# Performance work log

Hardware: AMD Instinct MI355X
Metric: run time of the kernel (lower is better)

The kernel has to match this reference:

```python
import jax, jax.numpy as jnp
import numpy as np

N = 100000          # nodes
E = 800000          # edges per relation
R = 6               # relations
B = 1000            # graphs
IN_DIM = 14
POS_COL = 5
PE = 8              # pos_emb_dim
H = 128             # hidden_dim
OUT = 128           # out_dim
NPOS = 24
D1 = IN_DIM - 1 + PE  # 21, GAT layer-1 input dim


def setup_inputs() -> dict:
    key = jax.random.key(0)
    ks = jax.random.split(key, 20)
    x_all = jax.random.normal(ks[0], (N, IN_DIM), dtype=jnp.float32)
    pos = jax.random.randint(ks[1], (N,), 0, NPOS)
    x_all = x_all.at[:, POS_COL].set(pos.astype(jnp.float32))
    edges = jax.random.randint(ks[2], (R, 2, E), 0, N, dtype=jnp.int32)
    batch = jnp.sort(jax.random.randint(ks[3], (N,), 0, B, dtype=jnp.int32))
    pos_table = jax.random.normal(ks[4], (NPOS, PE), dtype=jnp.float32) * 0.02
    W1 = jax.random.normal(ks[5], (R, D1, H), dtype=jnp.float32) * 0.1
    as1 = jax.random.normal(ks[6], (R, H), dtype=jnp.float32) * 0.1
    ad1 = jax.random.normal(ks[7], (R, H), dtype=jnp.float32) * 0.1
    b1 = jnp.zeros((R, H), dtype=jnp.float32)
    W2 = jax.random.normal(ks[8], (R, H, H), dtype=jnp.float32) * 0.05
    as2 = jax.random.normal(ks[9], (R, H), dtype=jnp.float32) * 0.1
    ad2 = jax.random.normal(ks[10], (R, H), dtype=jnp.float32) * 0.1
    b2 = jnp.zeros((R, H), dtype=jnp.float32)
    n1w = jnp.ones((H,), dtype=jnp.float32)
    n1b = jnp.zeros((H,), dtype=jnp.float32)
    n2w = jnp.ones((H,), dtype=jnp.float32)
    n2b = jnp.zeros((H,), dtype=jnp.float32)
    query = jax.random.normal(ks[11], (H,), dtype=jnp.float32) * 0.02
    projW = jax.random.normal(ks[12], (H, OUT), dtype=jnp.float32) * 0.05
    projb = jnp.zeros((OUT,), dtype=jnp.float32)
    return dict(x_all=x_all, edges=edges, batch=batch, pos_table=pos_table,
                W1=W1, as1=as1, ad1=ad1, b1=b1, W2=W2, as2=as2, ad2=ad2, b2=b2,
                n1w=n1w, n1b=n1b, n2w=n2w, n2b=n2b, query=query, projW=projW, projb=projb)


def _seg_softmax(logits, seg, num):
    m = jax.lax.stop_gradient(jax.ops.segment_max(logits, seg, num_segments=num))
    e = jnp.exp(logits - m[seg])
    s = jax.ops.segment_sum(e, seg, num_segments=num)
    return e / s[seg]


def _gat_layer(x, W, a_s, a_d, b, edges):
    # sum over R relation-specific GATConv(heads=1, concat=False) outputs
    n = x.shape[0]
    out = jnp.zeros((n, W.shape[-1]), dtype=x.dtype)
    for r in range(R):
        xp = x @ W[r]                       # [N, H] projected features
        src, dst = edges[r, 0], edges[r, 1]
        z = (xp @ a_s[r])[src] + (xp @ a_d[r])[dst]
        z = jnp.where(z > 0, z, 0.2 * z)    # LeakyReLU(0.2)
        alpha = _seg_softmax(z, dst, n)     # per-destination softmax
        agg = jax.ops.segment_sum(alpha[:, None] * xp[src], dst, num_segments=n)
        out = out + agg + b[r]
    return out


def _ln(x, w, b):
    mu = x.mean(-1, keepdims=True)
    v = ((x - mu) ** 2).mean(-1, keepdims=True)
    return (x - mu) / jnp.sqrt(v + 1e-5) * w + b


def reference(x_all, edges, batch, pos_table, W1, as1, ad1, b1,
              W2, as2, ad2, b2, n1w, n1b, n2w, n2b, query, projW, projb):
    cont = jnp.concatenate([x_all[:, :POS_COL], x_all[:, POS_COL + 1:]], axis=1)
    pidx = jnp.clip(x_all[:, POS_COL].astype(jnp.int32), 0, NPOS - 1)
    x = jnp.concatenate([cont, pos_table[pidx]], axis=1)  # [N, D1]
    x = _gat_layer(x, W1, as1, ad1, b1, edges)
    x = _ln(jax.nn.gelu(x, approximate=False), n1w, n1b)
    x = _gat_layer(x, W2, as2, ad2, b2, edges)
    x = _ln(jax.nn.gelu(x, approximate=False), n2w, n2b)
    # AttentionPooling: gather-score-softmax-scatter over batch segments
    scores = x @ query
    w = _seg_softmax(scores, batch, B)
    pool = jax.ops.segment_sum(w[:, None] * x, batch, num_segments=B)  # [B, H]
    return pool @ projW + projb
```

## Files before the change

kernel.cpp:

```cpp
#include <hip/hip_runtime.h>
#include <math.h>

#define NN   100000
#define EE   800000
#define RR   6
#define BB   1000
#define HH   128
#define MM   (RR*NN)
#define NBPR ((NN + 255) >> 8)
#define NBK  (RR * NBPR)
#define CH   4096
#define CAP  4096

static inline int ceil_div(int a, int b){ return (a+b-1)/b; }

typedef __attribute__((ext_vector_type(8))) short bf16x8;
typedef __attribute__((ext_vector_type(4))) short bf16x4;
typedef __attribute__((ext_vector_type(4))) float f32x4;

__device__ __forceinline__ unsigned fenc(float f){
  unsigned u = __float_as_uint(f);
  return (u & 0x80000000u) ? ~u : (u | 0x80000000u);
}
__device__ __forceinline__ float fdec(unsigned u){
  return __uint_as_float((u & 0x80000000u) ? (u & 0x7fffffffu) : ~u);
}
__device__ __forceinline__ unsigned short f2bf(float f){
  unsigned u = __float_as_uint(f);
  return (unsigned short)((u + 0x7fffu + ((u >> 16) & 1u)) >> 16);
}
__device__ __forceinline__ float bf2f(unsigned short h){
  return __uint_as_float(((unsigned)h) << 16);
}

__global__ void k_binscatter(const int* __restrict__ edges, int* __restrict__ bcur,
                             unsigned* __restrict__ ebkt)
{
  __shared__ int hist[NBPR];
  __shared__ int base[NBPR];
  int t = threadIdx.x;
  const int nch = (EE + CH - 1) / CH;
  int r = blockIdx.x / nch, c = blockIdx.x - r*nch;
  for (int i = t; i < NBPR; i += 256) hist[i] = 0;
  __syncthreads();
  const int* sptr = edges + (size_t)r*2*EE;
  const int* dptr = sptr + EE;
  int e0 = c*CH, e1 = min(EE, e0 + CH);
  for (int i = e0 + t; i < e1; i += 256)
    atomicAdd(&hist[dptr[i] >> 8], 1);
  __syncthreads();
  for (int i = t; i < NBPR; i += 256) {
    int h = hist[i];
    int gb = r*NBPR + i;
    base[i] = h ? (gb*CAP + atomicAdd(&bcur[gb], h)) : 0;
    hist[i] = 0;
  }
  __syncthreads();
  for (int i = e0 + t; i < e1; i += 256) {
    int dst = dptr[i];
    int b = dst >> 8;
    int slot = base[b] + atomicAdd(&hist[b], 1);
    ebkt[slot] = ((unsigned)sptr[i] << 8) | (unsigned)(dst & 255);
  }
}

__global__ void k_bscan(const int* __restrict__ bcur, int* __restrict__ boff,
                        int* __restrict__ off)
{
  __shared__ int sh[256];
  int t = threadIdx.x;
  int carry = 0;
  for (int c = 0; c < NBK; c += 256) {
    int idx = c + t;
    int v = (idx < NBK) ? bcur[idx] : 0;
    sh[t] = v;
    __syncthreads();
    for (int o = 1; o < 256; o <<= 1) {
      int add = (t >= o) ? sh[t-o] : 0;
      __syncthreads();
      sh[t] += add;
      __syncthreads();
    }
    int incl = sh[t];
    int tot  = sh[255];
    if (idx < NBK) boff[idx] = carry + incl - v;
    __syncthreads();
    carry += tot;
  }
  if (t == 0) { boff[NBK] = carry; off[MM] = carry; }
}

__global__ void k_bbuild(const unsigned* __restrict__ ebkt, const int* __restrict__ bcur,
                         const int* __restrict__ boff,
                         int* __restrict__ off, int* __restrict__ elist)
{
  __shared__ int cnt[256];
  __shared__ int sc[256];
  __shared__ int cur[256];
  int t = threadIdx.x;
  int bb = blockIdx.x;
  int e0r = bb*CAP, e1r = e0r + bcur[bb];
  int w0 = boff[bb];
  cnt[t] = 0;
  __syncthreads();
  for (int i = e0r + t; i < e1r; i += 256)
    atomicAdd(&cnt[ebkt[i] & 255u], 1);
  __syncthreads();
  sc[t] = cnt[t];
  __syncthreads();
  for (int o = 1; o < 256; o <<= 1) {
    int add = (t >= o) ? sc[t-o] : 0;
    __syncthreads();
    sc[t] += add;
    __syncthreads();
  }
  int excl = sc[t] - cnt[t];
  int r = bb / NBPR, b = bb - r*NBPR;
  int dst = b*256 + t;
  if (dst < NN) off[r*NN + dst] = w0 + excl;
  cur[t] = w0 + excl;
  __syncthreads();
  for (int i = e0r + t; i < e1r; i += 256) {
    unsigned w = ebkt[i];
    int slot = atomicAdd(&cur[w & 255u], 1);
    elist[slot] = (int)(w >> 8);
  }
}

__global__ void k_featprep(const float* __restrict__ x_all, const float* __restrict__ pos_table,
                           short* __restrict__ x0h, short* __restrict__ x0l)
{
  int gid = blockIdx.x*256 + threadIdx.x;
  if (gid >= NN*32) return;
  int nidx = gid >> 5, c = gid & 31;
  float v = 0.f;
  if (c < 13) {
    int scl = (c < 5) ? c : c + 1;
    v = x_all[nidx*14 + scl];
  } else if (c < 21) {
    int pi = (int)x_all[nidx*14 + 5];
    pi = pi < 0 ? 0 : (pi > 23 ? 23 : pi);
    v = pos_table[pi*8 + (c - 13)];
  }
  unsigned short h = f2bf(v);
  unsigned short l = f2bf(v - bf2f(h));
  x0h[gid] = (short)h;
  x0l[gid] = (short)l;
}

template<int KP>
__global__ void k_wprep(const float* __restrict__ W, int K,
                        short* __restrict__ Wh, short* __restrict__ Wl)
{
  int gid = blockIdx.x*256 + threadIdx.x;
  if (gid >= RR*128*KP) return;
  int r = gid / (128*KP);
  int rem = gid - r*(128*KP);
  int nn = rem / KP, k = rem - nn*KP;
  float v = (k < K) ? W[((size_t)r*K + k)*128 + nn] : 0.f;
  unsigned short h = f2bf(v);
  unsigned short l = f2bf(v - bf2f(h));
  Wh[gid] = (short)h;
  Wl[gid] = (short)l;
}

__global__ void k_wprep2(const float* __restrict__ W,
                         short* __restrict__ Wh, short* __restrict__ Wl)
{
  int gid = blockIdx.x*256 + threadIdx.x;
  if (gid >= RR*128*128) return;
  int r = gid / (128*128);
  int i = gid - r*(128*128);
  int kc = i >> 12;
  int lg = (i >> 10) & 3;
  int row = (i >> 3) & 127;
  int e = i & 7;
  int k = kc*32 + 16*(e >> 2) + 4*lg + (e & 3);
  float v = W[((size_t)r*128 + k)*128 + row];
  unsigned short h = f2bf(v);
  unsigned short l = f2bf(v - bf2f(h));
  Wh[gid] = (short)h;
  Wl[gid] = (short)l;
}

template<int KP>
__global__ void k_wa(const float* __restrict__ W, const float* __restrict__ as,
                     const float* __restrict__ ad, int K, float* __restrict__ wa)
{
  int idx = blockIdx.x*256 + threadIdx.x;
  if (idx >= 12*KP) return;
  int rr = idx / KP, k = idx - rr*KP;
  int r = (rr < 6) ? rr : rr - 6;
  const float* a = ((rr < 6) ? as : ad) + (size_t)r*HH;
  float s = 0.f;
  if (k < K) {
    const float* wrow = W + ((size_t)r*K + k)*128;
    #pragma unroll 8
    for (int h = 0; h < 128; ++h) s = fmaf(wrow[h], a[h], s);
  }
  wa[idx] = s;
}

__global__ void k_zsd32(const short* __restrict__ xh, const short* __restrict__ xl,
                        const float* __restrict__ wa, float* __restrict__ zsd, int n)
{
  __shared__ float w[12*32];
  int tid = threadIdx.x;
  for (int i = tid; i < 12*32; i += 256) w[i] = wa[i];
  __syncthreads();
  int g = blockIdx.x*256 + tid;
  if (g >= n) return;
  float v[32];
  #pragma unroll
  for (int c = 0; c < 4; ++c) {
    uint4 vh = *(const uint4*)(xh + (size_t)g*32 + c*8);
    uint4 vl = *(const uint4*)(xl + (size_t)g*32 + c*8);
    const unsigned short* hp = (const unsigned short*)&vh;
    const unsigned short* lp = (const unsigned short*)&vl;
    #pragma unroll
    for (int j = 0; j < 8; ++j) v[c*8+j] = bf2f(hp[j]) + bf2f(lp[j]);
  }
  #pragma unroll
  for (int rr = 0; rr < 12; ++rr) {
    float d = 0.f;
    #pragma unroll
    for (int k = 0; k < 32; ++k) d = fmaf(v[k], w[rr*32+k], d);
    zsd[(size_t)rr*n + g] = d;
  }
}

__global__ void k_zsd128(const unsigned short* __restrict__ xh,
                         const float* __restrict__ wa, float* __restrict__ zsd, int n)
{
  __shared__ float w[12*128];
  int tid = threadIdx.x;
  for (int i = tid; i < 12*128; i += 256) w[i] = wa[i];
  __syncthreads();
  int gid = blockIdx.x*256 + tid;
  int g = gid >> 4, l = tid & 15;
  if (g >= n) return;
  uint4 vh = *(const uint4*)(xh + (size_t)g*128 + l*8);
  const unsigned short* hp = (const unsigned short*)&vh;
  float v[8];
  #pragma unroll
  for (int j = 0; j < 8; ++j) v[j] = bf2f(hp[j]);
  float dot[12];
  #pragma unroll
  for (int rr = 0; rr < 12; ++rr) {
    float p = 0.f;
    #pragma unroll
    for (int j = 0; j < 8; ++j) p = fmaf(v[j], w[rr*128 + l*8 + j], p);
    p += __shfl_xor(p, 1); p += __shfl_xor(p, 2);
    p += __shfl_xor(p, 4); p += __shfl_xor(p, 8);
    dot[rr] = p;
  }
  if (l < 12) zsd[(size_t)l*n + g] = dot[l];
}

__global__ void k_agg1(const unsigned short* __restrict__ x0h, const float* __restrict__ zsd,
                       const int* __restrict__ elist, const int* __restrict__ off,
                       unsigned short* __restrict__ aggH, unsigned short* __restrict__ aggL,
                       int n)
{
  int gid = blockIdx.x*256 + threadIdx.x;
  int g = gid >> 4;
  int l = threadIdx.x & 15;
  if (g >= n) return;
  int sub = l >> 2, ch = l & 3;

  for (int rel = 0; rel < RR; ++rel) {
    const float* zsr = zsd + (size_t)rel*n;
    const float* zdr = zsd + (size_t)(6+rel)*n;
    int o0 = off[(size_t)rel*NN + g];
    int deg = off[(size_t)rel*NN + g + 1] - o0;
    float acc[8] = {0,0,0,0,0,0,0,0};
    float inv = 0.f;
    if (deg > 0) {
      float zdd = zdr[g];
      float m = -3.4e38f, es = 0.f;
      for (int i = l; i < deg; i += 16) {
        float z = zsr[elist[o0+i]] + zdd;
        z = (z > 0.f) ? z : 0.2f*z;
        float mn = fmaxf(m, z);
        es = es*__expf(m - mn) + __expf(z - mn);
        m = mn;
      }
      #pragma unroll
      for (int o = 1; o <= 8; o <<= 1) {
        float mo = __shfl_xor(m, o), eo = __shfl_xor(es, o);
        float mn = fmaxf(m, mo);
        es = es*__expf(m - mn) + eo*__expf(mo - mn);
        m = mn;
      }
      inv = 1.f / es;
      for (int base = 0; base < deg; base += 8) {
        int i0 = base + sub, i1 = base + 4 + sub;
        float e0 = 0.f, e1 = 0.f; int s0 = 0, s1 = 0;
        if (i0 < deg) {
          s0 = elist[o0+i0];
          float z = zsr[s0] + zdd;
          z = (z > 0.f) ? z : 0.2f*z;
          e0 = __expf(z - m);
        }
        if (i1 < deg) {
          s1 = elist[o0+i1];
          float z = zsr[s1] + zdd;
          z = (z > 0.f) ? z : 0.2f*z;
          e1 = __expf(z - m);
        }
        uint4 v0 = *(const uint4*)(x0h + (size_t)s0*32 + ch*8);
        uint4 v1 = *(const uint4*)(x0h + (size_t)s1*32 + ch*8);
        acc[0] = fmaf(e0, __uint_as_float(v0.x << 16),         acc[0]);
        acc[1] = fmaf(e0, __uint_as_float(v0.x & 0xffff0000u), acc[1]);
        acc[2] = fmaf(e0, __uint_as_float(v0.y << 16),         acc[2]);
        acc[3] = fmaf(e0, __uint_as_float(v0.y & 0xffff0000u), acc[3]);
        acc[4] = fmaf(e0, __uint_as_float(v0.z << 16),         acc[4]);
        acc[5] = fmaf(e0, __uint_as_float(v0.z & 0xffff0000u), acc[5]);
        acc[6] = fmaf(e0, __uint_as_float(v0.w << 16),         acc[6]);
        acc[7] = fmaf(e0, __uint_as_float(v0.w & 0xffff0000u), acc[7]);
        acc[0] = fmaf(e1, __uint_as_float(v1.x << 16),         acc[0]);
        acc[1] = fmaf(e1, __uint_as_float(v1.x & 0xffff0000u), acc[1]);
        acc[2] = fmaf(e1, __uint_as_float(v1.y << 16),         acc[2]);
        acc[3] = fmaf(e1, __uint_as_float(v1.y & 0xffff0000u), acc[3]);
        acc[4] = fmaf(e1, __uint_as_float(v1.z << 16),         acc[4]);
        acc[5] = fmaf(e1, __uint_as_float(v1.z & 0xffff0000u), acc[5]);
        acc[6] = fmaf(e1, __uint_as_float(v1.w << 16),         acc[6]);
        acc[7] = fmaf(e1, __uint_as_float(v1.w & 0xffff0000u), acc[7]);
      }
      #pragma unroll
      for (int j = 0; j < 8; ++j) {
        acc[j] += __shfl_xor(acc[j], 4);
        acc[j] += __shfl_xor(acc[j], 8);
      }
    }
    if (sub == 0) {
      uint4 ph, pl;
      unsigned* php = (unsigned*)&ph; unsigned* plp = (unsigned*)&pl;
      #pragma unroll
      for (int j2 = 0; j2 < 4; ++j2) {
        float a0 = acc[2*j2]   * inv;
        float a1 = acc[2*j2+1] * inv;
        unsigned short h0 = f2bf(a0), h1 = f2bf(a1);
        php[j2] = ((unsigned)h1 << 16) | h0;
        plp[j2] = ((unsigned)f2bf(a1 - bf2f(h1)) << 16) | f2bf(a0 - bf2f(h0));
      }
      size_t o = ((size_t)rel*n + g)*32 + ch*8;
      *(uint4*)(aggH + o) = ph;
      *(uint4*)(aggL + o) = pl;
    }
  }
}

__device__ __forceinline__ bf16x8 ldfragG(const short* __restrict__ p, int row, int kb, int KP_)
{
  bf16x4 a = *(const bf16x4*)(p + (size_t)row*KP_ + kb);
  bf16x4 b = *(const bf16x4*)(p + (size_t)row*KP_ + kb + 16);
  return __builtin_shufflevector(a, b, 0,1,2,3,4,5,6,7);
}

__global__ __launch_bounds__(256, 4)
void k_gemm1(const short* __restrict__ aggH, const short* __restrict__ aggL,
             const short* __restrict__ Wh, const short* __restrict__ Wl,
             const float* __restrict__ bsv,
             const float* __restrict__ nw, const float* __restrict__ nb,
             unsigned short* __restrict__ Yh, int n)
{
  __shared__ __align__(16) float Cs[32*136];
  int tid = threadIdx.x;
  int r0 = blockIdx.x * 32;
  int wid = tid >> 6, lane = tid & 63;
  int lr = lane & 15, lg = lane >> 4;
  int rt = wid >> 1;
  int c0 = (wid & 1) * 4;
  int arow = r0 + rt*16 + lr;
  int kb = 4*lg;
  f32x4 acct[4] = {{0,0,0,0},{0,0,0,0},{0,0,0,0},{0,0,0,0}};

  for (int rel = 0; rel < RR; ++rel) {
    const short* Ahr = aggH + (size_t)rel*n*32;
    const short* Alr = aggL + (size_t)rel*n*32;
    const short* Whr = Wh + (size_t)rel*128*32;
    const short* Wlr = Wl + (size_t)rel*128*32;
    bf16x8 ah = ldfragG(Ahr, arow, kb, 32);
    bf16x8 al = ldfragG(Alr, arow, kb, 32);
    #pragma unroll
    for (int t = 0; t < 4; ++t) {
      int wrow = (c0 + t)*16 + lr;
      bf16x8 whf = ldfragG(Whr, wrow, kb, 32);
      bf16x8 wlf = ldfragG(Wlr, wrow, kb, 32);
      acct[t] = __builtin_amdgcn_mfma_f32_16x16x32_bf16(ah, whf, acct[t], 0, 0, 0);
      acct[t] = __builtin_amdgcn_mfma_f32_16x16x32_bf16(al, whf, acct[t], 0, 0, 0);
      acct[t] = __builtin_amdgcn_mfma_f32_16x16x32_bf16(ah, wlf, acct[t], 0, 0, 0);
    }
  }

  #pragma unroll
  for (int t = 0; t < 4; ++t)
    #pragma unroll
    for (int v = 0; v < 4; ++v) {
      int row = rt*16 + lg*4 + v;
      int col = (c0 + t)*16 + lr;
      float x = acct[t][v] + bsv[col];
      Cs[row*136 + col] = 0.5f*x*(1.f + erff(x*0.70710678118654752f));
    }
  __syncthreads();
  {
    int r = tid >> 3, sg = tid & 7;
    float vals[16];
    float s = 0.f;
    #pragma unroll
    for (int i = 0; i < 16; ++i) { vals[i] = Cs[r*136 + sg*16 + i]; s += vals[i]; }
    s += __shfl_xor(s, 1); s += __shfl_xor(s, 2); s += __shfl_xor(s, 4);
    float mu = s * (1.f/128.f);
    float var = 0.f;
    #pragma unroll
    for (int i = 0; i < 16; ++i) { vals[i] -= mu; var += vals[i]*vals[i]; }
    var += __shfl_xor(var, 1); var += __shfl_xor(var, 2); var += __shfl_xor(var, 4);
    float inv = 1.f / sqrtf(var*(1.f/128.f) + 1e-5f);
    int g = r0 + r;
    uint4 ph0, ph1;
    unsigned* php0 = (unsigned*)&ph0; unsigned* php1 = (unsigned*)&ph1;
    #pragma unroll
    for (int j2 = 0; j2 < 8; ++j2) {
      int c = sg*16 + 2*j2;
      float y0 = vals[2*j2]  *inv*nw[c]   + nb[c];
      float y1 = vals[2*j2+1]*inv*nw[c+1] + nb[c+1];
      unsigned hw = ((unsigned)f2bf(y1) << 16) | f2bf(y0);
      if (j2 < 4) php0[j2] = hw; else php1[j2-4] = hw;
    }
    *(uint4*)(Yh + (size_t)g*128 + sg*16)     = ph0;
    *(uint4*)(Yh + (size_t)g*128 + sg*16 + 8) = ph1;
  }
}

#define ACC8(W_, U_) \
  tmp[0] = fmaf(W_, __uint_as_float((U_).x << 16),         tmp[0]); \
  tmp[1] = fmaf(W_, __uint_as_float((U_).x & 0xffff0000u), tmp[1]); \
  tmp[2] = fmaf(W_, __uint_as_float((U_).y << 16),         tmp[2]); \
  tmp[3] = fmaf(W_, __uint_as_float((U_).y & 0xffff0000u), tmp[3]); \
  tmp[4] = fmaf(W_, __uint_as_float((U_).z << 16),         tmp[4]); \
  tmp[5] = fmaf(W_, __uint_as_float((U_).z & 0xffff0000u), tmp[5]); \
  tmp[6] = fmaf(W_, __uint_as_float((U_).w << 16),         tmp[6]); \
  tmp[7] = fmaf(W_, __uint_as_float((U_).w & 0xffff0000u), tmp[7]);

__global__ void k_agg2(const unsigned short* __restrict__ h1,
                       const float* __restrict__ zsd,
                       const int* __restrict__ elist,
                       const int* __restrict__ off,
                       int rbase,
                       unsigned short* __restrict__ agg2,
                       int n)
{
  int gid = blockIdx.x*256 + threadIdx.x;
  int g = gid >> 4;
  int l = threadIdx.x & 15;
  int gbase = threadIdx.x & 48;
  if (g >= n) return;

  for (int r = 0; r < 3; ++r) {
    int o0 = off[(size_t)r*NN + g], o1 = off[(size_t)r*NN + g + 1];
    int deg = o1 - o0;
    float tmp[8] = {0,0,0,0,0,0,0,0};
    float inv = 0.f;
    if (deg > 0) {
      const float* zsr = zsd + (size_t)(rbase+r)*n;
      float zdd = zsd[(size_t)(6+rbase+r)*n + g];

      float m = -3.4e38f;
      for (int i = l; i < deg; i += 16) {
        float z = zsr[elist[o0+i]] + zdd;
        z = (z > 0.f) ? z : 0.2f*z;
        m = fmaxf(m, z);
      }
      m = fmaxf(m, __shfl_xor(m, 1));
      m = fmaxf(m, __shfl_xor(m, 2));
      m = fmaxf(m, __shfl_xor(m, 4));
      m = fmaxf(m, __shfl_xor(m, 8));

      float esum = 0.f;
      for (int base = 0; base < deg; base += 16) {
        int i = base + l;
        float ew = 0.f; int s = 0;
        if (i < deg) {
          s = elist[o0+i];
          float z = zsr[s] + zdd;
          z = (z > 0.f) ? z : 0.2f*z;
          ew = __expf(z - m);
        }
        esum += ew;
        int cnt = min(16, deg - base);
        for (int t = 0; t < cnt; t += 4) {
          float w0 = __shfl(ew, gbase + t);
          float w1 = __shfl(ew, gbase + t + 1);
          float w2 = __shfl(ew, gbase + t + 2);
          float w3 = __shfl(ew, gbase + t + 3);
          int a0 = __shfl(s, gbase + t);
          int a1 = __shfl(s, gbase + t + 1);
          int a2 = __shfl(s, gbase + t + 2);
          int a3 = __shfl(s, gbase + t + 3);
          uint4 u0 = *(const uint4*)(h1 + (size_t)a0*128 + l*8);
          uint4 u1 = *(const uint4*)(h1 + (size_t)a1*128 + l*8);
          uint4 u2 = *(const uint4*)(h1 + (size_t)a2*128 + l*8);
          uint4 u3 = *(const uint4*)(h1 + (size_t)a3*128 + l*8);
          ACC8(w0, u0);
          ACC8(w1, u1);
          ACC8(w2, u2);
          ACC8(w3, u3);
        }
      }
      esum += __shfl_xor(esum, 1);
      esum += __shfl_xor(esum, 2);
      esum += __shfl_xor(esum, 4);
      esum += __shfl_xor(esum, 8);
      inv = 1.f / esum;
    }
    uint4 ph;
    unsigned* php = (unsigned*)&ph;
    #pragma unroll
    for (int j2 = 0; j2 < 4; ++j2) {
      float a0 = tmp[2*j2]   * inv;
      float a1 = tmp[2*j2+1] * inv;
      php[j2] = ((unsigned)f2bf(a1) << 16) | f2bf(a0);
    }
    *(uint4*)(agg2 + ((size_t)r*n + g)*128 + l*8) = ph;
  }
}

template<int FIN>
__global__ __launch_bounds__(512, 2)
void k_gemm2(const unsigned short* __restrict__ agg2,
             const short* __restrict__ WhAll, const short* __restrict__ WlAll, int rbase,
             const float* __restrict__ bsv,
             const float* __restrict__ nw, const float* __restrict__ nb,
             float* __restrict__ hacc, float* __restrict__ Yf,
             const float* __restrict__ q, const int* __restrict__ batch,
             float* __restrict__ scores, unsigned* __restrict__ bmax, int n)
{
  constexpr int KP = 128;
  __shared__ __align__(16) short lds[2*128*KP];
  constexpr int WH0 = 0, WL0 = 128*KP;
  int tid = threadIdx.x;
  int r0 = blockIdx.x * 128;
  int wid = tid >> 6, lane = tid & 63;
  int lr = lane & 15, lg = lane >> 4;
  int grow = r0 + wid*16 + lr;
  int growc = min(grow, n-1);
  f32x4 acc[8] = {{0,0,0,0},{0,0,0,0},{0,0,0,0},{0,0,0,0},
                  {0,0,0,0},{0,0,0,0},{0,0,0,0},{0,0,0,0}};

  for (int rel = 0; rel < 3; ++rel) {
    const short* Ar = (const short*)(agg2 + (size_t)rel*n*KP);
    const short* Wh = WhAll + (size_t)(rbase+rel)*128*KP;
    const short* Wl = WlAll + (size_t)(rbase+rel)*128*KP;
    for (int ch = tid; ch < 128*16; ch += 512) {
      *(bf16x8*)(lds + WH0 + ch*8) = *(const bf16x8*)(Wh + (size_t)ch*8);
      *(bf16x8*)(lds + WL0 + ch*8) = *(const bf16x8*)(Wl + (size_t)ch*8);
    }
    __syncthreads();
    #pragma unroll
    for (int kc = 0; kc < 4; ++kc) {
      int kb = kc*32 + 4*lg;
      bf16x8 ah = ldfragG(Ar, growc, kb, KP);
      int fbase = ((kc*4 + lg)*128)*8;
      #pragma unroll
      for (int ct = 0; ct < 8; ++ct) {
        int wrow = ct*16 + lr;
        bf16x8 wh = *(const bf16x8*)(lds + WH0 + fbase + wrow*8);
        bf16x8 wl = *(const bf16x8*)(lds + WL0 + fbase + wrow*8);
        acc[ct] = __builtin_amdgcn_mfma_f32_16x16x32_bf16(ah, wh, acc[ct], 0, 0, 0);
        acc[ct] = __builtin_amdgcn_mfma_f32_16x16x32_bf16(ah, wl, acc[ct], 0, 0, 0);
      }
    }
    __syncthreads();
  }

  if (FIN == 0) {
    #pragma unroll
    for (int v = 0; v < 4; ++v) {
      int row = r0 + wid*16 + lg*4 + v;
      if (row < n) {
        #pragma unroll
        for (int ct = 0; ct < 8; ++ct)
          hacc[(size_t)row*128 + ct*16 + lr] = acc[ct][v];
      }
    }
  } else {
    #pragma unroll
    for (int v = 0; v < 4; ++v) {
      int row = r0 + wid*16 + lg*4 + v;
      int rowc = min(row, n-1);
      float vals[8];
      float s = 0.f;
      #pragma unroll
      for (int ct = 0; ct < 8; ++ct) {
        int c = ct*16 + lr;
        float x = acc[ct][v] + hacc[(size_t)rowc*128 + c] + bsv[c];
        x = 0.5f*x*(1.f + erff(x*0.70710678118654752f));
        vals[ct] = x;
        s += x;
      }
      s += __shfl_xor(s, 1); s += __shfl_xor(s, 2);
      s += __shfl_xor(s, 4); s += __shfl_xor(s, 8);
      float mu = s * (1.f/128.f);
      float var = 0.f;
      #pragma unroll
      for (int ct = 0; ct < 8; ++ct) { vals[ct] -= mu; var += vals[ct]*vals[ct]; }
      var += __shfl_xor(var, 1); var += __shfl_xor(var, 2);
      var += __shfl_xor(var, 4); var += __shfl_xor(var, 8);
      float inv = 1.f / sqrtf(var*(1.f/128.f) + 1e-5f);
      float sc = 0.f;
      #pragma unroll
      for (int ct = 0; ct < 8; ++ct) {
        int c = ct*16 + lr;
        float y = vals[ct]*inv*nw[c] + nb[c];
        if (row < n) Yf[(size_t)row*128 + c] = y;
        sc = fmaf(y, q[c], sc);
      }
      sc += __shfl_xor(sc, 1); sc += __shfl_xor(sc, 2);
      sc += __shfl_xor(sc, 4); sc += __shfl_xor(sc, 8);
      if (lr == 0 && row < n) {
        scores[row] = sc;
        atomicMax(&bmax[batch[row]], fenc(sc));
      }
    }
  }
}

__global__ void k_bsum(const float* __restrict__ b, float* __restrict__ bs)
{
  int t = threadIdx.x;
  float s = 0.f;
  #pragma unroll
  for (int r = 0; r < RR; ++r) s += b[r*HH + t];
  bs[t] = s;
}

__global__ void k_segbounds(const int* __restrict__ batch, int* __restrict__ segst,
                            int n, int numB)
{
  int b = blockIdx.x*256 + threadIdx.x;
  if (b > numB) return;
  int lo = 0, hi = n;
  while (lo < hi) { int mid = (lo+hi) >> 1; if (batch[mid] < b) lo = mid+1; else hi = mid; }
  segst[b] = lo;
}

__global__ void k_pool(const float* __restrict__ X, const float* __restrict__ scores,
                       const int* __restrict__ segst, const unsigned* __restrict__ bmax,
                       float* __restrict__ pool, int numB)
{
  int b = blockIdx.x;
  int t = threadIdx.x;
  int s0 = segst[b], s1 = segst[b+1];
  float m = fdec(bmax[b]);
  float acc0 = 0.f, acc1 = 0.f, esum = 0.f;
  int i = s0;
  for (; i + 1 < s1; i += 2) {
    float e0 = __expf(scores[i] - m);
    float e1 = __expf(scores[i+1] - m);
    esum += e0 + e1;
    acc0 = fmaf(e0, X[(size_t)i*128 + t], acc0);
    acc1 = fmaf(e1, X[(size_t)(i+1)*128 + t], acc1);
  }
  if (i < s1) {
    float e0 = __expf(scores[i] - m);
    esum += e0;
    acc0 = fmaf(e0, X[(size_t)i*128 + t], acc0);
  }
  float inv = (s1 > s0) ? 1.f/esum : 0.f;
  pool[(size_t)b*128 + t] = (acc0 + acc1) * inv;
}

__global__ void k_outgemm(const float* __restrict__ pool, const float* __restrict__ projW,
                          const float* __restrict__ projb, float* __restrict__ out, int numB)
{
  int b = blockIdx.x;
  int j = threadIdx.x;
  __shared__ float p[128];
  p[j] = pool[(size_t)b*128 + j];
  __syncthreads();
  float acc = projb[j];
  #pragma unroll 16
  for (int k = 0; k < 128; ++k) acc = fmaf(p[k], projW[(size_t)k*128 + j], acc);
  out[(size_t)b*128 + j] = acc;
}

extern "C" void kernel_launch(void* const* d_in, const int* in_sizes, int n_in,
                              void* d_out, int out_size, void* d_ws, size_t ws_size,
                              hipStream_t stream)
{
  const float* x_all = (const float*)d_in[0];
  const int*   edges = (const int*)d_in[1];
  const int*   batch = (const int*)d_in[2];
  const float* pos_table = (const float*)d_in[3];
  const float* W1  = (const float*)d_in[4];
  const float* as1 = (const float*)d_in[5];
  const float* ad1 = (const float*)d_in[6];
  const float* b1  = (const float*)d_in[7];
  const float* W2  = (const float*)d_in[8];
  const float* as2 = (const float*)d_in[9];
  const float* ad2 = (const float*)d_in[10];
  const float* b2  = (const float*)d_in[11];
  const float* n1w = (const float*)d_in[12];
  const float* n1b = (const float*)d_in[13];
  const float* n2w = (const float*)d_in[14];
  const float* n2b = (const float*)d_in[15];
  const float* query = (const float*)d_in[16];
  const float* projW = (const float*)d_in[17];
  const float* projb = (const float*)d_in[18];
  float* out = (float*)d_out;
  (void)in_sizes; (void)n_in; (void)out_size; (void)ws_size;

  char* p = (char*)d_ws;
  auto alloc = [&](size_t b){ void* r = (void*)p; p += (b + 255) & ~(size_t)255; return r; };
  int*   off   = (int*)alloc((size_t)(MM+1)*sizeof(int));
  int*   elist = (int*)alloc((size_t)RR*EE*sizeof(int));
  int*   boff  = (int*)alloc((size_t)(NBK+1)*sizeof(int));
  int*   bcur  = (int*)alloc((size_t)NBK*sizeof(int));
  short* wtH   = (short*)alloc((size_t)RR*128*128*sizeof(short));
  short* wtL   = (short*)alloc((size_t)RR*128*128*sizeof(short));
  float* wa    = (float*)alloc((size_t)12*128*sizeof(float));
  float* zsd   = (float*)alloc((size_t)12*NN*sizeof(float));
  float* bsv   = (float*)alloc(128*sizeof(float));
  int*   segst = (int*)alloc((size_t)(BB+1)*sizeof(int));
  unsigned* bmax = (unsigned*)alloc((size_t)BB*sizeof(unsigned));
  float* pool  = (float*)alloc((size_t)BB*HH*sizeof(float));
  float* scrs  = (float*)alloc((size_t)NN*sizeof(float));
  unsigned short* big = (unsigned short*)alloc((size_t)3*NN*128*sizeof(short));
  float* R1    = (float*)alloc((size_t)NN*128*sizeof(float));
  float* R2    = (float*)alloc((size_t)NN*128*sizeof(float));

  unsigned* ebkt = (unsigned*)R1;
  short* x0h = (short*)R1;
  short* x0l = x0h + (size_t)NN*32;
  float* hacc = R1;
  unsigned short* h1h = (unsigned short*)R2;
  float* h2 = (float*)R2;
  unsigned short* aggH = big;
  unsigned short* aggL = aggH + (size_t)RR*NN*32;
  unsigned short* agg2 = big;

  const int nch = (EE + CH - 1) / CH;
  hipMemsetAsync(bcur, 0, (size_t)NBK*sizeof(int), stream);
  k_binscatter<<<RR*nch,256,0,stream>>>(edges, bcur, ebkt);
  k_bscan<<<1,256,0,stream>>>(bcur, boff, off);
  k_bbuild<<<NBK,256,0,stream>>>(ebkt, bcur, boff, off, elist);

  k_featprep<<<ceil_div(NN*32,256),256,0,stream>>>(x_all, pos_table, x0h, x0l);
  k_segbounds<<<ceil_div(BB+1,256),256,0,stream>>>(batch, segst, NN, BB);
  hipMemsetAsync(bmax, 0, (size_t)BB*sizeof(unsigned), stream);

  k_wa<32><<<ceil_div(12*32,256),256,0,stream>>>(W1, as1, ad1, 21, wa);
  k_zsd32<<<ceil_div(NN,256),256,0,stream>>>(x0h, x0l, wa, zsd, NN);
  k_wprep<32><<<ceil_div(RR*128*32,256),256,0,stream>>>(W1, 21, wtH, wtL);
  k_bsum<<<1,128,0,stream>>>(b1, bsv);
  k_agg1<<<ceil_div(NN*16,256),256,0,stream>>>((const unsigned short*)x0h, zsd, elist, off,
                                               aggH, aggL, NN);
  k_gemm1<<<ceil_div(NN,32),256,0,stream>>>((const short*)aggH, (const short*)aggL,
                                            wtH, wtL, bsv, n1w, n1b, h1h, NN);

  k_wa<128><<<ceil_div(12*128,256),256,0,stream>>>(W2, as2, ad2, 128, wa);
  k_zsd128<<<ceil_div(NN*16,256),256,0,stream>>>(h1h, wa, zsd, NN);
  k_wprep2<<<ceil_div(RR*128*128,256),256,0,stream>>>(W2, wtH, wtL);
  k_bsum<<<1,128,0,stream>>>(b2, bsv);
  int aggGrid = ceil_div(NN*16, 256);
  int gemm2Grid = ceil_div(NN, 128);
  k_agg2<<<aggGrid,256,0,stream>>>(h1h, zsd, elist, off, 0, agg2, NN);
  k_gemm2<0><<<gemm2Grid,512,0,stream>>>(agg2, wtH, wtL, 0, bsv, n2w, n2b,
      hacc, (float*)0, query, batch, scrs, bmax, NN);
  k_agg2<<<aggGrid,256,0,stream>>>(h1h, zsd, elist, off + (size_t)3*NN, 3, agg2, NN);
  k_gemm2<1><<<gemm2Grid,512,0,stream>>>(agg2, wtH, wtL, 3, bsv, n2w, n2b,
      hacc, h2, query, batch, scrs, bmax, NN);

  k_pool<<<BB,128,0,stream>>>(h2, scrs, segst, bmax, pool, BB);
  k_outgemm<<<BB,128,0,stream>>>(pool, projW, projb, out, BB);
}
```

Before: 782.7 us.

## Drop softmax max pass with clamped exp and single-bf16 layer-1 aggregates

Replaces the per-destination max pre-pass in both aggregation kernels with a clamped exponent (a LeakyReLU'd logit clipped to ±60), so each edge list is read once instead of twice. It also drops the low-order bf16 residual of the layer-1 aggregates, which removes one output stream and one MFMA per tile in gemm1. The risks are reduced precision in the layer-1 GEMM input and a departure from exact softmax stabilisation if logits ever exceed the clamp range.

```diff
diff --git a/kernel.cpp b/kernel.cpp
--- a/kernel.cpp
+++ b/kernel.cpp
@@ -31,6 +31,11 @@
 }
 __device__ __forceinline__ float bf2f(unsigned short h){
   return __uint_as_float(((unsigned)h) << 16);
+}
+__device__ __forceinline__ float wexp(float z){
+  z = (z > 0.f) ? z : 0.2f*z;
+  z = fminf(fmaxf(z, -60.f), 60.f);
+  return __expf(z);
 }
 
 __global__ void k_binscatter(const int* __restrict__ edges, int* __restrict__ bcur,
@@ -259,8 +264,7 @@
 
 __global__ void k_agg1(const unsigned short* __restrict__ x0h, const float* __restrict__ zsd,
                        const int* __restrict__ elist, const int* __restrict__ off,
-                       unsigned short* __restrict__ aggH, unsigned short* __restrict__ aggL,
-                       int n)
+                       unsigned short* __restrict__ aggH, int n)
 {
   int gid = blockIdx.x*256 + threadIdx.x;
   int g = gid >> 4;
@@ -274,40 +278,22 @@
     int o0 = off[(size_t)rel*NN + g];
     int deg = off[(size_t)rel*NN + g + 1] - o0;
     float acc[8] = {0,0,0,0,0,0,0,0};
+    float esum = 0.f;
     float inv = 0.f;
     if (deg > 0) {
       float zdd = zdr[g];
-      float m = -3.4e38f, es = 0.f;
-      for (int i = l; i < deg; i += 16) {
-        float z = zsr[elist[o0+i]] + zdd;
-        z = (z > 0.f) ? z : 0.2f*z;
-        float mn = fmaxf(m, z);
-        es = es*__expf(m - mn) + __expf(z - mn);
-        m = mn;
-      }
-      #pragma unroll
-      for (int o = 1; o <= 8; o <<= 1) {
-        float mo = __shfl_xor(m, o), eo = __shfl_xor(es, o);
-        float mn = fmaxf(m, mo);
-        es = es*__expf(m - mn) + eo*__expf(mo - mn);
-        m = mn;
-      }
-      inv = 1.f / es;
       for (int base = 0; base < deg; base += 8) {
         int i0 = base + sub, i1 = base + 4 + sub;
         float e0 = 0.f, e1 = 0.f; int s0 = 0, s1 = 0;
         if (i0 < deg) {
           s0 = elist[o0+i0];
-          float z = zsr[s0] + zdd;
-          z = (z > 0.f) ? z : 0.2f*z;
-          e0 = __expf(z - m);
+          e0 = wexp(zsr[s0] + zdd);
         }
         if (i1 < deg) {
           s1 = elist[o0+i1];
-          float z = zsr[s1] + zdd;
-          z = (z > 0.f) ? z : 0.2f*z;
-          e1 = __expf(z - m);
+          e1 = wexp(zsr[s1] + zdd);
         }
+        esum += e0 + e1;
         uint4 v0 = *(const uint4*)(x0h + (size_t)s0*32 + ch*8);
         uint4 v1 = *(const uint4*)(x0h + (size_t)s1*32 + ch*8);
         acc[0] = fmaf(e0, __uint_as_float(v0.x << 16),         acc[0]);
@@ -327,26 +313,25 @@
         acc[6] = fmaf(e1, __uint_as_float(v1.w << 16),         acc[6]);
         acc[7] = fmaf(e1, __uint_as_float(v1.w & 0xffff0000u), acc[7]);
       }
+      esum += __shfl_xor(esum, 4);
+      esum += __shfl_xor(esum, 8);
       #pragma unroll
       for (int j = 0; j < 8; ++j) {
         acc[j] += __shfl_xor(acc[j], 4);
         acc[j] += __shfl_xor(acc[j], 8);
       }
+      inv = 1.f / esum;
     }
     if (sub == 0) {
-      uint4 ph, pl;
-      unsigned* php = (unsigned*)&ph; unsigned* plp = (unsigned*)&pl;
+      uint4 ph;
+      unsigned* php = (unsigned*)&ph;
       #pragma unroll
       for (int j2 = 0; j2 < 4; ++j2) {
         float a0 = acc[2*j2]   * inv;
         float a1 = acc[2*j2+1] * inv;
-        unsigned short h0 = f2bf(a0), h1 = f2bf(a1);
-        php[j2] = ((unsigned)h1 << 16) | h0;
-        plp[j2] = ((unsigned)f2bf(a1 - bf2f(h1)) << 16) | f2bf(a0 - bf2f(h0));
-      }
-      size_t o = ((size_t)rel*n + g)*32 + ch*8;
-      *(uint4*)(aggH + o) = ph;
-      *(uint4*)(aggL + o) = pl;
+        php[j2] = ((unsigned)f2bf(a1) << 16) | f2bf(a0);
+      }
+      *(uint4*)(aggH + ((size_t)rel*n + g)*32 + ch*8) = ph;
     }
   }
 }
@@ -359,7 +344,7 @@
 }
 
 __global__ __launch_bounds__(256, 4)
-void k_gemm1(const short* __restrict__ aggH, const short* __restrict__ aggL,
+void k_gemm1(const short* __restrict__ aggH,
              const short* __restrict__ Wh, const short* __restrict__ Wl,
              const float* __restrict__ bsv,
              const float* __restrict__ nw, const float* __restrict__ nb,
@@ -378,18 +363,15 @@
 
   for (int rel = 0; rel < RR; ++rel) {
     const short* Ahr = aggH + (size_t)rel*n*32;
-    const short* Alr = aggL + (size_t)rel*n*32;
     const short* Whr = Wh + (size_t)rel*128*32;
     const short* Wlr = Wl + (size_t)rel*128*32;
     bf16x8 ah = ldfragG(Ahr, arow, kb, 32);
-    bf16x8 al = ldfragG(Alr, arow, kb, 32);
     #pragma unroll
     for (int t = 0; t < 4; ++t) {
       int wrow = (c0 + t)*16 + lr;
       bf16x8 whf = ldfragG(Whr, wrow, kb, 32);
       bf16x8 wlf = ldfragG(Wlr, wrow, kb, 32);
       acct[t] = __builtin_amdgcn_mfma_f32_16x16x32_bf16(ah, whf, acct[t], 0, 0, 0);
-      acct[t] = __builtin_amdgcn_mfma_f32_16x16x32_bf16(al, whf, acct[t], 0, 0, 0);
       acct[t] = __builtin_amdgcn_mfma_f32_16x16x32_bf16(ah, wlf, acct[t], 0, 0, 0);
     }
   }
@@ -465,27 +447,13 @@
     if (deg > 0) {
       const float* zsr = zsd + (size_t)(rbase+r)*n;
       float zdd = zsd[(size_t)(6+rbase+r)*n + g];
-
-      float m = -3.4e38f;
-      for (int i = l; i < deg; i += 16) {
-        float z = zsr[elist[o0+i]] + zdd;
-        z = (z > 0.f) ? z : 0.2f*z;
-        m = fmaxf(m, z);
-      }
-      m = fmaxf(m, __shfl_xor(m, 1));
-      m = fmaxf(m, __shfl_xor(m, 2));
-      m = fmaxf(m, __shfl_xor(m, 4));
-      m = fmaxf(m, __shfl_xor(m, 8));
-
       float esum = 0.f;
       for (int base = 0; base < deg; base += 16) {
         int i = base + l;
         float ew = 0.f; int s = 0;
         if (i < deg) {
           s = elist[o0+i];
-          float z = zsr[s] + zdd;
-          z = (z > 0.f) ? z : 0.2f*z;
-          ew = __expf(z - m);
+          ew = wexp(zsr[s] + zdd);
         }
         esum += ew;
         int cnt = min(16, deg - base);
@@ -737,7 +705,6 @@
   unsigned short* h1h = (unsigned short*)R2;
   float* h2 = (float*)R2;
   unsigned short* aggH = big;
-  unsigned short* aggL = aggH + (size_t)RR*NN*32;
   unsigned short* agg2 = big;
 
   const int nch = (EE + CH - 1) / CH;
@@ -755,8 +722,8 @@
   k_wprep<32><<<ceil_div(RR*128*32,256),256,0,stream>>>(W1, 21, wtH, wtL);
   k_bsum<<<1,128,0,stream>>>(b1, bsv);
   k_agg1<<<ceil_div(NN*16,256),256,0,stream>>>((const unsigned short*)x0h, zsd, elist, off,
-                                               aggH, aggL, NN);
-  k_gemm1<<<ceil_div(NN,32),256,0,stream>>>((const short*)aggH, (const short*)aggL,
+                                               aggH, NN);
+  k_gemm1<<<ceil_div(NN,32),256,0,stream>>>((const short*)aggH,
                                             wtH, wtL, bsv, n1w, n1b, h1h, NN);
 
   k_wa<128><<<ceil_div(12*128,256),256,0,stream>>>(W2, as2, ad2, 128, wa);
```

Result: faster. 740.6 us, median of 2 (-5.4%).
